# Performance work log

Hardware: AMD Instinct MI355X
Metric: run time of the kernel (lower is better)

Reference implementation:

```python
import jax, jax.numpy as jnp
import numpy as np

# dims
N = 32768      # nodes
E = 1048576    # edges (avg degree 32)
DIN = 64       # input scalar dim
NS = 64        # 0e multiplicity of hidden irreps
NV = 32        # 1o multiplicity of hidden irreps
LAT = 256      # config.LATENT_DIM_GNN
L = 2          # n_layers
S3 = 1.0 / np.sqrt(3.0)  # CG coefficient for 1o x 1o -> 0e (dot / sqrt(3))


def setup_inputs() -> dict:
    key = jax.random.key(0)
    ks = jax.random.split(key, 20)
    p = lambda k, s: jax.random.normal(k, s, jnp.float32)
    return {
        "x": p(ks[0], (N, DIN)),
        "edge_attr": p(ks[2], (E, 4)),            # [rel_vec(3) | dist(1)] = 1x1o + 1x0e
        "W_in": p(ks[3], (DIN, NS)),              # initial e3nn Linear: only 0e->0e connects
        "W_out": p(ks[4], (NS, LAT)),             # final projection on scalar irreps
        "W_ss": p(ks[5], (L, NS, NS)),            # message TP: 0e x 0e -> 0e
        "W_vv0": p(ks[6], (L, NV, NS)),           # message TP: 1o x 1o -> 0e
        "W_sv": p(ks[7], (L, NS, NV)),            # message TP: 0e x 1o -> 1o
        "W_vs": p(ks[8], (L, NV, NV)),            # message TP: 1o x 0e -> 1o
        "gm_w": p(ks[9], (L, NV * 3)), "gm_b": p(ks[10], (L, NV * 3)),
        "W_uss": p(ks[11], (L, NS, NS, NS)),      # update TP: 0e x 0e -> 0e
        "W_uvv": p(ks[12], (L, NV, NV, NS)),      # update TP: 1o x 1o -> 0e
        "W_usv": p(ks[13], (L, NS, NV, NV)),      # update TP: 0e x 1o -> 1o
        "W_uvs": p(ks[14], (L, NV, NS, NV)),      # update TP: 1o x 0e -> 1o
        "gu_w": p(ks[15], (L, NV * 3)), "gu_b": p(ks[16], (L, NV * 3)),
        "edge_index": jax.random.randint(ks[1], (2, E), 0, N),
    }


def _gate(s, v, gw, gb):
    # RobustGate manual path: silu on scalars; vectors gated by
    # sigmoid(Linear(mean over nonscalar dims)) broadcast over the flattened block.
    s = jax.nn.silu(s)
    vf = v.reshape(v.shape[0], -1)                       # [*, NV*3]
    g = jax.nn.sigmoid(vf.mean(-1, keepdims=True) * gw + gb)
    return s, (vf * g).reshape(v.shape)


def reference(x, edge_attr, W_in, W_out, W_ss, W_vv0, W_sv, W_vs, gm_w, gm_b,
              W_uss, W_uvv, W_usv, W_uvs, gu_w, gu_b, edge_index):
    row, col = edge_index[0], edge_index[1]
    ev, es = edge_attr[:, :3], edge_attr[:, 3]           # 1x1o, 1x0e edge attrs
    # initial projection 64x0e -> 64x0e + 32x1o (vector part starts at zero)
    ns = x @ W_in / np.sqrt(DIN)                         # [N, NS]
    nv = jnp.zeros((x.shape[0], NV, 3), x.dtype)         # [N, NV, 3]
    r2 = np.sqrt(2.0)
    for l in range(L):
        # ---- message: gather -> FullyConnectedTensorProduct(node, edge) ----
        hs, hv = ns[col], nv[col]
        m_s = (jnp.einsum('ei,io->eo', hs * es[:, None], W_ss[l]) / np.sqrt(NS)
               + jnp.einsum('emx,ex,mo->eo', hv, ev, W_vv0[l]) * S3 / np.sqrt(NV)) / r2
        m_v = (jnp.einsum('ei,ex,im->emx', hs, ev, W_sv[l]) / np.sqrt(NS)
               + jnp.einsum('emx,mn->enx', hv * es[:, None, None], W_vs[l]) / np.sqrt(NV)) / r2
        m_s, m_v = _gate(m_s, m_v, gm_w[l], gm_b[l])
        # ---- scatter-add aggregation ----
        a_s = jax.ops.segment_sum(m_s, row, num_segments=N)
        a_v = jax.ops.segment_sum(m_v, row, num_segments=N)
        # ---- update: FullyConnectedTensorProduct(node, aggregated) ----
        u_s = (jnp.einsum('ei,ej,ijo->eo', ns, a_s, W_uss[l]) / NS
               + jnp.einsum('emx,enx,mno->eo', nv, a_v, W_uvv[l]) * S3 / NV) / r2
        u_v = (jnp.einsum('ei,enx,ino->eox', ns, a_v, W_usv[l]) / np.sqrt(NS * NV)
               + jnp.einsum('emx,ej,mjo->eox', nv, a_s, W_uvs[l]) / np.sqrt(NS * NV)) / r2
        u_s, u_v = _gate(u_s, u_v, gu_w[l], gu_b[l])
        # residual node update
        ns = ns + u_s
        nv = nv + u_v
    # extract scalar (l=0) features, final projection to LAT x 0e
    return ns @ W_out / np.sqrt(NS)
```

## Files before the change

kernel.cpp:

```cpp
#include <hip/hip_runtime.h>

#define N_NODES 32768
#define N_EDGES 1048576
#define PREP_L  467968

typedef short bfrag8 __attribute__((ext_vector_type(8)));
typedef float f32x4  __attribute__((ext_vector_type(4)));

#define MFMA(a,b,c) __builtin_amdgcn_mfma_f32_16x16x32_bf16(a,b,c,0,0,0)

__device__ __forceinline__ short f2bf(float f){
    unsigned u = __float_as_uint(f);
    u += 0x7fffu + ((u >> 16) & 1u);
    return (short)(u >> 16);
}
__device__ __forceinline__ float bf2f(short s){
    return __uint_as_float(((unsigned)(unsigned short)s) << 16);
}
__device__ __forceinline__ float sigm(float x){ return 1.0f/(1.0f + __expf(-x)); }
__device__ __forceinline__ float siluf(float x){ return x * sigm(x); }

__global__ void k_prep(const float* Wss, const float* Wvv0, const float* Wsv,
                       const float* Wvs, const float* Wuss, const float* Wuvv,
                       const float* Wusv, const float* Wuvs, const float* Wout,
                       short* wp)
{
    int idx = blockIdx.x*256 + threadIdx.x;
    const int total = 2*PREP_L + 16384;
    if (idx >= total) return;
    const float s_ss  = 0.0883883476483f;
    const float s_vv  = 0.0721687836487f;
    const float s_sv  = 0.0883883476483f;
    const float s_vs  = 0.125f;
    const float s_uss = 0.0110485434560f;
    const float s_uvv = 0.0127577593310f;
    const float s_uvw = 0.015625f;
    float v;
    if (idx >= 2*PREP_L){
        int r = idx - 2*PREP_L; int o = r >> 6, i = r & 63;
        v = Wout[i*256 + o] * 0.125f;
    } else {
        int l = idx / PREP_L; int off = idx - l*PREP_L;
        if (off < 6144){ int o = off/96, k = off - o*96;
            v = (k < 64) ? Wss[l*4096 + k*64 + o]*s_ss
                         : Wvv0[l*2048 + (k-64)*64 + o]*s_vv;
        } else if (off < 8192){ int tt = off - 6144; int m = tt>>6, i = tt&63;
            v = Wsv[l*2048 + i*32 + m]*s_sv;
        } else if (off < 9216){ int tt = off - 8192; int n = tt>>5, m = tt&31;
            v = Wvs[l*1024 + m*32 + n]*s_vs;
        } else if (off < 336896){ int tt = off - 9216; int o = tt/5120, k = tt - o*5120;
            if (k < 4096) v = Wuss[l*262144 + k*64 + o]*s_uss;
            else          v = Wuvv[l*65536 + (k-4096)*64 + o]*s_uvv;
        } else if (off < 402432){ int tt = off - 336896; int nf = tt>>6, i = tt&63;
            int n = nf>>5, o = nf&31;
            v = Wusv[l*65536 + i*1024 + n*32 + o]*s_uvw;
        } else { int tt = off - 402432; int nf = tt>>6, j = tt&63;
            int m = nf>>5, o = nf&31;
            v = Wuvs[l*65536 + m*2048 + j*32 + o]*s_uvw;
        }
    }
    wp[idx] = f2bf(v);
}

__global__ void k_in(const float* __restrict__ x, const float* __restrict__ Win,
                     float* __restrict__ ns)
{
    int wv = threadIdx.x >> 6, o = threadIdx.x & 63;
    int node = blockIdx.x*4 + wv;
    const float* xr = x + (size_t)node*64;
    float acc = 0.f;
    #pragma unroll
    for (int i=0;i<64;i++) acc += xr[i]*Win[i*64+o];
    ns[(size_t)node*64+o] = 0.125f*acc;
}

__global__ void k_pack(const float* __restrict__ ns, const float* __restrict__ nv,
                       short* __restrict__ nsbf, short* __restrict__ nvbf)
{
    int t = threadIdx.x;
    int nb = blockIdx.x*16;
    for (int idx=t; idx<1024; idx+=256){
        int nd = idx>>6, i = idx&63;
        nsbf[(size_t)(nb+nd)*64 + i] = f2bf(ns[(size_t)(nb+nd)*64 + i]);
    }
    for (int idx=t; idx<1536; idx+=256){
        int nd = idx/96, r = idx - nd*96;
        int x = r>>5, m = r&31;
        nvbf[((size_t)x<<20) + (size_t)(nb+nd)*32 + m] = f2bf(nv[(size_t)(nb+nd)*96 + m*3 + x]);
    }
}

__global__ void k_hist(const int* __restrict__ eidx, int* __restrict__ cnt)
{
    int e = blockIdx.x*256 + threadIdx.x;
    atomicAdd(&cnt[eidx[e]], 1);
}

__global__ void k_scan(const int* __restrict__ cnt, int* __restrict__ cursor)
{
    __shared__ int part[256];
    int t = threadIdx.x;
    int base = t*128;
    int s = 0;
    for (int i=0;i<128;i++) s += cnt[base+i];
    part[t] = s; __syncthreads();
    for (int off=1; off<256; off<<=1){
        int v = (t>=off) ? part[t-off] : 0;
        __syncthreads();
        part[t] += v;
        __syncthreads();
    }
    int run = part[t] - s;
    for (int i=0;i<128;i++){ cursor[base+i] = run; run += cnt[base+i]; }
}

__global__ void k_scatter(const int* __restrict__ eidx, const float* __restrict__ eattr,
                          int* __restrict__ cursor, int* __restrict__ col_s,
                          int* __restrict__ row_s, float4* __restrict__ ea_s)
{
    int e = blockIdx.x*256 + threadIdx.x;
    int r = eidx[e];
    int d = atomicAdd(&cursor[r], 1);
    row_s[d] = r;
    col_s[d] = eidx[N_EDGES + e];
    ea_s[d]  = ((const float4*)eattr)[e];
}

__global__ __launch_bounds__(256, 3) void k_edge(
        const short* __restrict__ nsbf, const short* __restrict__ nvbf,
        const int* __restrict__ col_s, const int* __restrict__ row_s,
        const float4* __restrict__ ea_s,
        const short* __restrict__ wp_l,
        const float* __restrict__ gmw, const float* __restrict__ gmb,
        float* __restrict__ a_s, float* __restrict__ a_v)
{
    __shared__ __align__(16) short sA1[4][16*36];
    __shared__ __align__(16) short sA2[4][16*72];
    __shared__ __align__(16) short sAv[4][3*16*36];
    __shared__ int    sRow[4][16];
    __shared__ float4 sEv4[4][16];
    __shared__ float  sAcc[24*160];

    const int t = threadIdx.x;
    const int w = t >> 6, lane = t & 63;
    const int col = lane & 15, quad = lane >> 4;
    const int blockStart = blockIdx.x*256;
    const int rfirst = row_s[blockStart];

    for (int i=t; i<24*160; i+=256) sAcc[i] = 0.f;

    const short* W1t  = wp_l;
    const short* Wsvt = wp_l + 6144;
    const short* Wvst = wp_l + 8192;

    bfrag8 bss[2][4], bvv[4], bsv[2][2], bvs[2];
    #pragma unroll
    for (int s=0;s<2;s++)
        #pragma unroll
        for (int nt=0;nt<4;nt++)
            bss[s][nt] = *(const bfrag8*)(W1t + (nt*16+col)*96 + s*32 + quad*8);
    #pragma unroll
    for (int nt=0;nt<4;nt++)
        bvv[nt] = *(const bfrag8*)(W1t + (nt*16+col)*96 + 64 + quad*8);
    #pragma unroll
    for (int s=0;s<2;s++)
        #pragma unroll
        for (int nt=0;nt<2;nt++)
            bsv[s][nt] = *(const bfrag8*)(Wsvt + (nt*16+col)*64 + s*32 + quad*8);
    #pragma unroll
    for (int nt=0;nt<2;nt++)
        bvs[nt] = *(const bfrag8*)(Wvst + (nt*16+col)*32 + quad*8);

    float gwv[2][3], gbv[2][3];
    #pragma unroll
    for (int h=0;h<2;h++)
        #pragma unroll
        for (int xx=0;xx<3;xx++){
            int k = (h*16+col)*3+xx;
            gwv[h][xx] = gmw[k]; gbv[h][xx] = gmb[k];
        }

    auto emit = [&](int r, int f, float v){
        int rl = r - rfirst;
        if (rl < 24) atomicAdd(&sAcc[rl*160 + f], v);
        else if (f < 64) atomicAdd(&a_s[(size_t)r*64 + f], v);
        else             atomicAdd(&a_v[(size_t)r*96 + f - 64], v);
    };

    __syncthreads();

    for (int it=0; it<4; it++){
        int tileBase = blockStart + w*64 + it*16;
        {
            int e = col, q = quad;
            int sg = tileBase + e;
            int c = col_s[sg];
            float4 ea = ea_s[sg];
            const short* hsrc = nsbf + (size_t)c*64 + q*16;
            bfrag8 h0 = *(const bfrag8*)(hsrc);
            bfrag8 h1 = *(const bfrag8*)(hsrc + 8);
            *(bfrag8*)&sA2[w][e*72 + q*16]     = h0;
            *(bfrag8*)&sA2[w][e*72 + q*16 + 8] = h1;
            bfrag8 av[3];
            #pragma unroll
            for (int xx=0;xx<3;xx++){
                av[xx] = *(const bfrag8*)(nvbf + ((size_t)xx<<20) + (size_t)c*32 + q*8);
                *(bfrag8*)&sAv[w][xx*576 + e*36 + q*8] = av[xx];
            }
            bfrag8 vt;
            #pragma unroll
            for (int mi=0;mi<8;mi++)
                vt[mi] = f2bf(bf2f(av[0][mi])*ea.x + bf2f(av[1][mi])*ea.y + bf2f(av[2][mi])*ea.z);
            *(bfrag8*)&sA1[w][e*36 + q*8] = vt;
            if (q==0){
                sRow[w][e] = row_s[sg];
                sEv4[w][e] = ea;
            }
        }
        __syncthreads();
        f32x4 accss[4], accvv[4], accp[2], accq[3][2];
        #pragma unroll
        for (int nt=0;nt<4;nt++){ accss[nt] = (f32x4){0.f,0.f,0.f,0.f};
                                  accvv[nt] = (f32x4){0.f,0.f,0.f,0.f}; }
        #pragma unroll
        for (int nt=0;nt<2;nt++) accp[nt] = (f32x4){0.f,0.f,0.f,0.f};
        #pragma unroll
        for (int xx=0;xx<3;xx++)
            #pragma unroll
            for (int nt=0;nt<2;nt++) accq[xx][nt] = (f32x4){0.f,0.f,0.f,0.f};
        {
            bfrag8 a1 = *(bfrag8*)&sA1[w][col*36 + quad*8];
            bfrag8 a20 = *(bfrag8*)&sA2[w][col*72 + quad*8];
            bfrag8 a21 = *(bfrag8*)&sA2[w][col*72 + 32 + quad*8];
            #pragma unroll
            for (int nt=0;nt<4;nt++) accss[nt] = MFMA(a20, bss[0][nt], accss[nt]);
            #pragma unroll
            for (int nt=0;nt<4;nt++) accss[nt] = MFMA(a21, bss[1][nt], accss[nt]);
            #pragma unroll
            for (int nt=0;nt<4;nt++) accvv[nt] = MFMA(a1, bvv[nt], accvv[nt]);
            #pragma unroll
            for (int nt=0;nt<2;nt++) accp[nt] = MFMA(a20, bsv[0][nt], accp[nt]);
            #pragma unroll
            for (int nt=0;nt<2;nt++) accp[nt] = MFMA(a21, bsv[1][nt], accp[nt]);
            #pragma unroll
            for (int xx=0;xx<3;xx++){
                bfrag8 avx = *(bfrag8*)&sAv[w][xx*576 + col*36 + quad*8];
                #pragma unroll
                for (int nt=0;nt<2;nt++) accq[xx][nt] = MFMA(avx, bvs[nt], accq[xx][nt]);
            }
        }

        float4 ev4[4];
        #pragma unroll
        for (int reg=0;reg<4;reg++) ev4[reg] = sEv4[w][quad*4+reg];
        float mean[4];
        #pragma unroll
        for (int reg=0;reg<4;reg++){
            float es = ev4[reg].w;
            float part = 0.f;
            #pragma unroll
            for (int h=0;h<2;h++){
                part += accp[h][reg]*ev4[reg].x + es*accq[0][h][reg];
                part += accp[h][reg]*ev4[reg].y + es*accq[1][h][reg];
                part += accp[h][reg]*ev4[reg].z + es*accq[2][h][reg];
            }
            part += __shfl_xor(part,1); part += __shfl_xor(part,2);
            part += __shfl_xor(part,4); part += __shfl_xor(part,8);
            mean[reg] = part*(1.0f/96.0f);
        }

        int r0 = sRow[w][0], r15 = sRow[w][15];
        bool uni = (r0 == r15);
        int rq[4];
        #pragma unroll
        for (int reg=0;reg<4;reg++) rq[reg] = sRow[w][quad*4+reg];
        bool c1 = rq[1]==rq[0], c2 = rq[2]==rq[1], c3 = rq[3]==rq[2];
        auto out4 = [&](int f, float v0, float v1, float v2, float v3){
            if (uni){
                float s = v0+v1+v2+v3;
                s += __shfl_xor(s,16); s += __shfl_xor(s,32);
                if (quad==0) emit(r0, f, s);
            } else {
                float run = v0;
                if (c1) run += v1; else { emit(rq[0], f, run); run = v1; }
                if (c2) run += v2; else { emit(rq[1], f, run); run = v2; }
                if (c3) run += v3; else { emit(rq[2], f, run); run = v3; }
                emit(rq[3], f, run);
            }
        };
        #pragma unroll
        for (int nt=0;nt<4;nt++){
            float v[4];
            #pragma unroll
            for (int reg=0;reg<4;reg++)
                v[reg] = siluf(ev4[reg].w*accss[nt][reg] + accvv[nt][reg]);
            out4(nt*16+col, v[0], v[1], v[2], v[3]);
        }
        #pragma unroll
        for (int h=0;h<2;h++)
            #pragma unroll
            for (int xx=0;xx<3;xx++){
                float v[4];
                #pragma unroll
                for (int reg=0;reg<4;reg++){
                    float evx = (xx==0) ? ev4[reg].x : ((xx==1) ? ev4[reg].y : ev4[reg].z);
                    float val = accp[h][reg]*evx + ev4[reg].w*accq[xx][h][reg];
                    v[reg] = val * sigm(mean[reg]*gwv[h][xx] + gbv[h][xx]);
                }
                out4(64 + (h*16+col)*3+xx, v[0], v[1], v[2], v[3]);
            }
        __syncthreads();
    }

    int rlast = row_s[blockStart + 255];
    int nr = rlast - rfirst + 1; if (nr > 24) nr = 24;
    for (int i=t; i<nr*160; i+=256){
        float v = sAcc[i];
        if (v != 0.f){
            int rl = i/160, f = i - rl*160;
            int r = rfirst + rl;
            if (f < 64) atomicAdd(&a_s[(size_t)r*64 + f], v);
            else        atomicAdd(&a_v[(size_t)r*96 + f - 64], v);
        }
    }
}

__global__ __launch_bounds__(256) void k_us(
        const float* __restrict__ ns, const float* __restrict__ nvv,
        const float* __restrict__ a_s, const float* __restrict__ a_v,
        const short* __restrict__ Wusst, float* __restrict__ ns_out)
{
    __shared__ __align__(16) float ns16[16*68];
    __shared__ __align__(16) float as16[16*68];
    __shared__ __align__(16) float nv16[16*100];
    __shared__ __align__(16) float av16[16*100];
    __shared__ __align__(16) short sA[16*1032];

    const int t = threadIdx.x;
    const int w = t>>6, lane = t&63, col = lane&15, quad = lane>>4;
    const int nb = blockIdx.x*16;

    for (int idx=t; idx<1024; idx+=256){ int nd = idx>>6, i = idx&63;
        ns16[nd*68+i] = ns[(size_t)(nb+nd)*64+i];
        as16[nd*68+i] = a_s[(size_t)(nb+nd)*64+i];
    }
    for (int idx=t; idx<1536; idx+=256){ int nd = idx/96, i = idx-nd*96;
        nv16[nd*100+i] = nvv[(size_t)(nb+nd)*96+i];
        av16[nd*100+i] = a_v[(size_t)(nb+nd)*96+i];
    }
    __syncthreads();

    f32x4 acc = {0.f,0.f,0.f,0.f};
    for (int c=0;c<5;c++){
        if (c) __syncthreads();
        if (c < 4){
            #pragma unroll
            for (int itg=0; itg<8; itg++){
                int rid = t + itg*256;
                int nd = rid & 15;
                int kk0 = (rid>>4)<<3;
                int i = (c<<4) + (kk0>>6);
                int j0 = kk0 & 63;
                float nsv = ns16[nd*68 + i];
                const float* ap = &as16[nd*68 + j0];
                float4 x0 = *(const float4*)ap;
                float4 x1 = *(const float4*)(ap+4);
                bfrag8 o8;
                o8[0]=f2bf(nsv*x0.x); o8[1]=f2bf(nsv*x0.y); o8[2]=f2bf(nsv*x0.z); o8[3]=f2bf(nsv*x0.w);
                o8[4]=f2bf(nsv*x1.x); o8[5]=f2bf(nsv*x1.y); o8[6]=f2bf(nsv*x1.z); o8[7]=f2bf(nsv*x1.w);
                *(bfrag8*)&sA[nd*1032 + kk0] = o8;
            }
        } else {
            #pragma unroll
            for (int itg=0; itg<8; itg++){
                int rid = t + itg*256;
                int nd = rid & 15;
                int kk0 = (rid>>4)<<3;
                int m = kk0>>5, n0 = kk0&31;
                float v0 = nv16[nd*100 + m*3];
                float v1 = nv16[nd*100 + m*3+1];
                float v2 = nv16[nd*100 + m*3+2];
                const float* vp = &av16[nd*100 + n0*3];
                float yf[24];
                #pragma unroll
                for (int a=0;a<6;a++){ float4 y = *(const float4*)(vp+4*a);
                    yf[4*a]=y.x; yf[4*a+1]=y.y; yf[4*a+2]=y.z; yf[4*a+3]=y.w; }
                bfrag8 o8;
                #pragma unroll
                for (int jj=0;jj<8;jj++)
                    o8[jj] = f2bf(v0*yf[jj*3] + v1*yf[jj*3+1] + v2*yf[jj*3+2]);
                *(bfrag8*)&sA[nd*1032 + kk0] = o8;
            }
        }
        __syncthreads();
        const short* bp = Wusst + (size_t)(w*16+col)*5120 + c*1024 + quad*8;
        #pragma unroll
        for (int s=0;s<32;s++){
            bfrag8 a = *(bfrag8*)&sA[col*1032 + s*32 + quad*8];
            bfrag8 b = *(const bfrag8*)(bp + s*32);
            acc = MFMA(a, b, acc);
        }
    }
    #pragma unroll
    for (int reg=0; reg<4; reg++){
        int nd = quad*4 + reg;
        int o = w*16 + col;
        ns_out[(size_t)(nb+nd)*64 + o] = ns16[nd*68 + o] + siluf(acc[reg]);
    }
}

__global__ __launch_bounds__(256) void k_uv(
        const float* __restrict__ ns, const float* __restrict__ nvv,
        const float* __restrict__ a_s, const float* __restrict__ a_v,
        const short* __restrict__ Wusvt, const short* __restrict__ Wuvst,
        const float* __restrict__ guw, const float* __restrict__ gub,
        float* __restrict__ nv_out)
{
    __shared__ __align__(16) short nsbf[16*72];
    __shared__ __align__(16) short asbf[16*72];
    __shared__ __align__(16) float nv16[16*100];
    __shared__ __align__(16) float av16[16*100];
    __shared__ float uvb[2][16][96];

    const int t = threadIdx.x;
    const int w = t>>6, lane = t&63, col = lane&15, quad = lane>>4;
    const int nb = blockIdx.x*16;

    for (int idx=t; idx<1024; idx+=256){ int nd = idx>>6, i = idx&63;
        nsbf[nd*72+i] = f2bf(ns[(size_t)(nb+nd)*64+i]);
        asbf[nd*72+i] = f2bf(a_s[(size_t)(nb+nd)*64+i]);
    }
    for (int idx=t; idx<1536; idx+=256){ int nd = idx/96, i = idx-nd*96;
        nv16[nd*100+i] = nvv[(size_t)(nb+nd)*96+i];
        av16[nd*100+i] = a_v[(size_t)(nb+nd)*96+i];
    }
    __syncthreads();

    const int h = w>>1, o0 = (w&1)*16;
    const short* src = h ? asbf : nsbf;
    bfrag8 a0 = *(bfrag8*)&src[col*72 + quad*8];
    bfrag8 a1 = *(bfrag8*)&src[col*72 + 32 + quad*8];
    const short* Bt = h ? Wuvst : Wusvt;
    const float* M  = h ? nv16 : av16;
    float uva[3][4] = {};
    for (int n=0;n<32;n++){
        f32x4 acc = {0.f,0.f,0.f,0.f};
        const short* bp = Bt + (size_t)((n<<5) + o0 + col)*64 + quad*8;
        bfrag8 b0 = *(const bfrag8*)(bp);
        bfrag8 b1 = *(const bfrag8*)(bp + 32);
        acc = MFMA(a0,b0,acc);
        acc = MFMA(a1,b1,acc);
        #pragma unroll
        for (int reg=0;reg<4;reg++){
            int nd = quad*4+reg;
            float m0 = M[nd*100 + n*3];
            float m1 = M[nd*100 + n*3+1];
            float m2 = M[nd*100 + n*3+2];
            uva[0][reg] += acc[reg]*m0;
            uva[1][reg] += acc[reg]*m1;
            uva[2][reg] += acc[reg]*m2;
        }
    }
    #pragma unroll
    for (int reg=0;reg<4;reg++){
        int nd = quad*4+reg;
        #pragma unroll
        for (int xx=0;xx<3;xx++)
            uvb[h][nd][(o0+col)*3+xx] = uva[xx][reg];
    }
    __syncthreads();
    {
        int nd = t>>4, j = t&15;
        float part = 0.f;
        #pragma unroll
        for (int kk=j; kk<96; kk+=16) part += uvb[0][nd][kk] + uvb[1][nd][kk];
        part += __shfl_xor(part,1); part += __shfl_xor(part,2);
        part += __shfl_xor(part,4); part += __shfl_xor(part,8);
        float mean = part*(1.0f/96.0f);
        #pragma unroll
        for (int q2=0;q2<6;q2++){
            int kk = j*6 + q2;
            float uv = uvb[0][nd][kk] + uvb[1][nd][kk];
            float g = sigm(mean*guw[kk] + gub[kk]);
            nv_out[(size_t)(nb+nd)*96 + kk] = nv16[nd*100+kk] + uv*g;
        }
    }
}

__global__ __launch_bounds__(256) void k_out(const float* __restrict__ ns,
                                             const short* __restrict__ Woutt,
                                             float* __restrict__ outp)
{
    __shared__ __align__(16) short nsbf[16*72];
    const int t = threadIdx.x;
    const int w = t>>6, lane = t&63, col = lane&15, quad = lane>>4;
    const int nb = blockIdx.x*16;
    for (int idx=t; idx<1024; idx+=256){ int nd=idx>>6, i=idx&63;
        nsbf[nd*72+i] = f2bf(ns[(size_t)(nb+nd)*64+i]); }
    __syncthreads();
    bfrag8 a0 = *(bfrag8*)&nsbf[col*72 + quad*8];
    bfrag8 a1 = *(bfrag8*)&nsbf[col*72 + 32 + quad*8];
    #pragma unroll
    for (int nt=0;nt<4;nt++){
        int o = w*64 + nt*16 + col;
        const short* bp = Woutt + (size_t)o*64 + quad*8;
        bfrag8 b0 = *(const bfrag8*)bp;
        bfrag8 b1 = *(const bfrag8*)(bp+32);
        f32x4 acc = {0.f,0.f,0.f,0.f};
        acc = MFMA(a0,b0,acc);
        acc = MFMA(a1,b1,acc);
        #pragma unroll
        for (int reg=0;reg<4;reg++)
            outp[(size_t)(nb + quad*4+reg)*256 + o] = acc[reg];
    }
}

extern "C" void kernel_launch(void* const* d_in, const int* in_sizes, int n_in,
                              void* d_out, int out_size, void* d_ws, size_t ws_size,
                              hipStream_t stream)
{
    const float* x     = (const float*)d_in[0];
    const float* eattr = (const float*)d_in[1];
    const float* Win   = (const float*)d_in[2];
    const float* Wout  = (const float*)d_in[3];
    const float* Wss   = (const float*)d_in[4];
    const float* Wvv0  = (const float*)d_in[5];
    const float* Wsv   = (const float*)d_in[6];
    const float* Wvs   = (const float*)d_in[7];
    const float* gmw   = (const float*)d_in[8];
    const float* gmb   = (const float*)d_in[9];
    const float* Wuss  = (const float*)d_in[10];
    const float* Wuvv  = (const float*)d_in[11];
    const float* Wusv  = (const float*)d_in[12];
    const float* Wuvs  = (const float*)d_in[13];
    const float* guw   = (const float*)d_in[14];
    const float* gub   = (const float*)d_in[15];
    const int*   eidx  = (const int*)d_in[16];
    float* outp = (float*)d_out;

    char* p = (char*)d_ws;
    float* ns_a = (float*)p; p += (size_t)N_NODES*64*4;
    float* ns_b = (float*)p; p += (size_t)N_NODES*64*4;
    float* nv_a = (float*)p; p += (size_t)N_NODES*96*4;
    float* nv_b = (float*)p; p += (size_t)N_NODES*96*4;
    float* a_s  = (float*)p; p += (size_t)N_NODES*64*4;
    float* a_v  = (float*)p; p += (size_t)N_NODES*96*4;
    int*   cnt    = (int*)p;   p += (size_t)N_NODES*4;
    int*   cursor = (int*)p;   p += (size_t)N_NODES*4;
    int*   col_s  = (int*)p;   p += (size_t)N_EDGES*4;
    int*   row_s  = (int*)p;   p += (size_t)N_EDGES*4;
    float4* ea_s  = (float4*)p; p += (size_t)N_EDGES*16;
    short* wp   = (short*)p;   p += (size_t)(2*PREP_L + 16384)*2;
    short* nsbf = (short*)p;   p += (size_t)N_NODES*64*2;
    short* nvbf = (short*)p;   p += (size_t)3*N_NODES*32*2;

    k_prep<<<3720, 256, 0, stream>>>(Wss,Wvv0,Wsv,Wvs,Wuss,Wuvv,Wusv,Wuvs,Wout,wp);
    hipMemsetAsync(nv_a, 0, (size_t)N_NODES*96*4, stream);
    hipMemsetAsync(cnt, 0, (size_t)N_NODES*4, stream);
    k_in<<<N_NODES/4, 256, 0, stream>>>(x, Win, ns_a);
    k_hist<<<N_EDGES/256, 256, 0, stream>>>(eidx, cnt);
    k_scan<<<1, 256, 0, stream>>>(cnt, cursor);
    k_scatter<<<N_EDGES/256, 256, 0, stream>>>(eidx, eattr, cursor, col_s, row_s, ea_s);

    for (int l=0;l<2;l++){
        const float* cns = l ? ns_b : ns_a;
        const float* cnv = l ? nv_b : nv_a;
        float* nns = l ? ns_a : ns_b;
        float* nnv = l ? nv_a : nv_b;
        k_pack<<<N_NODES/16, 256, 0, stream>>>(cns, cnv, nsbf, nvbf);
        hipMemsetAsync(a_s, 0, (size_t)N_NODES*(64+96)*4, stream);
        k_edge<<<N_EDGES/256, 256, 0, stream>>>(nsbf, nvbf, col_s, row_s, ea_s,
                                         wp + (size_t)l*PREP_L,
                                         gmw + l*96, gmb + l*96, a_s, a_v);
        k_uv<<<N_NODES/16, 256, 0, stream>>>(cns, cnv, a_s, a_v,
                                             wp + (size_t)l*PREP_L + 336896,
                                             wp + (size_t)l*PREP_L + 402432,
                                             guw + l*96, gub + l*96, nnv);
        k_us<<<N_NODES/16, 256, 0, stream>>>(cns, cnv, a_s, a_v,
                                             wp + (size_t)l*PREP_L + 9216, nns);
    }
    k_out<<<N_NODES/16, 256, 0, stream>>>(ns_a, wp + (size_t)2*PREP_L, outp);
}
```

Baseline: 1.391 ms.

## Partition edge kernel by destination-node ranges via CSR row pointers, drop global atomics

The edge kernel now assigns each block a fixed range of 8 destination nodes, using a CSR row_ptr built in the scan kernel, instead of a fixed 256-edge chunk. All aggregation goes to shared memory and is written out once with plain stores, so the global atomics and the per-layer memset of a_s and a_v are no longer needed. The per-tile __syncthreads calls are removed because each wave only touches its own shared staging buffers. In exchange, per-block work now depends on node degree, so load can be uneven, and partial tiles need masking, which wastes some MFMA work on padded edges.

```diff
diff --git a/kernel.cpp b/kernel.cpp
--- a/kernel.cpp
+++ b/kernel.cpp
@@ -96,7 +96,8 @@
     atomicAdd(&cnt[eidx[e]], 1);
 }
 
-__global__ void k_scan(const int* __restrict__ cnt, int* __restrict__ cursor)
+__global__ void k_scan(const int* __restrict__ cnt, int* __restrict__ cursor,
+                       int* __restrict__ row_ptr)
 {
     __shared__ int part[256];
     int t = threadIdx.x;
@@ -111,7 +112,8 @@
         __syncthreads();
     }
     int run = part[t] - s;
-    for (int i=0;i<128;i++){ cursor[base+i] = run; run += cnt[base+i]; }
+    for (int i=0;i<128;i++){ cursor[base+i] = run; row_ptr[base+i] = run; run += cnt[base+i]; }
+    if (t == 255) row_ptr[N_NODES] = N_EDGES;
 }
 
 __global__ void k_scatter(const int* __restrict__ eidx, const float* __restrict__ eattr,
@@ -129,7 +131,7 @@
 __global__ __launch_bounds__(256, 3) void k_edge(
         const short* __restrict__ nsbf, const short* __restrict__ nvbf,
         const int* __restrict__ col_s, const int* __restrict__ row_s,
-        const float4* __restrict__ ea_s,
+        const float4* __restrict__ ea_s, const int* __restrict__ row_ptr,
         const short* __restrict__ wp_l,
         const float* __restrict__ gmw, const float* __restrict__ gmb,
         float* __restrict__ a_s, float* __restrict__ a_v)
@@ -139,15 +141,15 @@
     __shared__ __align__(16) short sAv[4][3*16*36];
     __shared__ int    sRow[4][16];
     __shared__ float4 sEv4[4][16];
-    __shared__ float  sAcc[24*160];
+    __shared__ float  sAcc[8*160];
 
     const int t = threadIdx.x;
     const int w = t >> 6, lane = t & 63;
     const int col = lane & 15, quad = lane >> 4;
-    const int blockStart = blockIdx.x*256;
-    const int rfirst = row_s[blockStart];
-
-    for (int i=t; i<24*160; i+=256) sAcc[i] = 0.f;
+    const int r0 = blockIdx.x*8;
+    const int e0 = row_ptr[r0], e1 = row_ptr[r0+8];
+
+    for (int i=t; i<8*160; i+=256) sAcc[i] = 0.f;
 
     const short* W1t  = wp_l;
     const short* Wsvt = wp_l + 6144;
@@ -180,22 +182,18 @@
             gwv[h][xx] = gmw[k]; gbv[h][xx] = gmb[k];
         }
 
-    auto emit = [&](int r, int f, float v){
-        int rl = r - rfirst;
-        if (rl < 24) atomicAdd(&sAcc[rl*160 + f], v);
-        else if (f < 64) atomicAdd(&a_s[(size_t)r*64 + f], v);
-        else             atomicAdd(&a_v[(size_t)r*96 + f - 64], v);
-    };
-
     __syncthreads();
 
-    for (int it=0; it<4; it++){
-        int tileBase = blockStart + w*64 + it*16;
+    const int ntiles = (e1 - e0 + 15) >> 4;
+    for (int tid=w; tid<ntiles; tid+=4){
         {
             int e = col, q = quad;
-            int sg = tileBase + e;
-            int c = col_s[sg];
-            float4 ea = ea_s[sg];
+            int sg = e0 + tid*16 + e;
+            bool valid = sg < e1;
+            int sgc = valid ? sg : (e1-1);
+            int c = col_s[sgc];
+            float4 ea = ea_s[sgc];
+            if (!valid){ ea.x=0.f; ea.y=0.f; ea.z=0.f; ea.w=0.f; }
             const short* hsrc = nsbf + (size_t)c*64 + q*16;
             bfrag8 h0 = *(const bfrag8*)(hsrc);
             bfrag8 h1 = *(const bfrag8*)(hsrc + 8);
@@ -213,11 +211,10 @@
                 vt[mi] = f2bf(bf2f(av[0][mi])*ea.x + bf2f(av[1][mi])*ea.y + bf2f(av[2][mi])*ea.z);
             *(bfrag8*)&sA1[w][e*36 + q*8] = vt;
             if (q==0){
-                sRow[w][e] = row_s[sg];
+                sRow[w][e] = row_s[sgc] - r0;
                 sEv4[w][e] = ea;
             }
         }
-        __syncthreads();
         f32x4 accss[4], accvv[4], accp[2], accq[3][2];
         #pragma unroll
         for (int nt=0;nt<4;nt++){ accss[nt] = (f32x4){0.f,0.f,0.f,0.f};
@@ -269,8 +266,8 @@
             mean[reg] = part*(1.0f/96.0f);
         }
 
-        int r0 = sRow[w][0], r15 = sRow[w][15];
-        bool uni = (r0 == r15);
+        int rl0 = sRow[w][0], rl15 = sRow[w][15];
+        bool uni = (rl0 == rl15);
         int rq[4];
         #pragma unroll
         for (int reg=0;reg<4;reg++) rq[reg] = sRow[w][quad*4+reg];
@@ -279,13 +276,13 @@
             if (uni){
                 float s = v0+v1+v2+v3;
                 s += __shfl_xor(s,16); s += __shfl_xor(s,32);
-                if (quad==0) emit(r0, f, s);
+                if (quad==0) atomicAdd(&sAcc[rl0*160 + f], s);
             } else {
                 float run = v0;
-                if (c1) run += v1; else { emit(rq[0], f, run); run = v1; }
-                if (c2) run += v2; else { emit(rq[1], f, run); run = v2; }
-                if (c3) run += v3; else { emit(rq[2], f, run); run = v3; }
-                emit(rq[3], f, run);
+                if (c1) run += v1; else { atomicAdd(&sAcc[rq[0]*160 + f], run); run = v1; }
+                if (c2) run += v2; else { atomicAdd(&sAcc[rq[1]*160 + f], run); run = v2; }
+                if (c3) run += v3; else { atomicAdd(&sAcc[rq[2]*160 + f], run); run = v3; }
+                atomicAdd(&sAcc[rq[3]*160 + f], run);
             }
         };
         #pragma unroll
@@ -309,19 +306,15 @@
                 }
                 out4(64 + (h*16+col)*3+xx, v[0], v[1], v[2], v[3]);
             }
-        __syncthreads();
-    }
-
-    int rlast = row_s[blockStart + 255];
-    int nr = rlast - rfirst + 1; if (nr > 24) nr = 24;
-    for (int i=t; i<nr*160; i+=256){
+    }
+
+    __syncthreads();
+    for (int i=t; i<8*160; i+=256){
+        int rl = i/160, f = i - rl*160;
+        int r = r0 + rl;
         float v = sAcc[i];
-        if (v != 0.f){
-            int rl = i/160, f = i - rl*160;
-            int r = rfirst + rl;
-            if (f < 64) atomicAdd(&a_s[(size_t)r*64 + f], v);
-            else        atomicAdd(&a_v[(size_t)r*96 + f - 64], v);
-        }
+        if (f < 64) a_s[(size_t)r*64 + f] = v;
+        else        a_v[(size_t)r*96 + f - 64] = v;
     }
 }
 
@@ -545,11 +538,12 @@
     float* nv_b = (float*)p; p += (size_t)N_NODES*96*4;
     float* a_s  = (float*)p; p += (size_t)N_NODES*64*4;
     float* a_v  = (float*)p; p += (size_t)N_NODES*96*4;
-    int*   cnt    = (int*)p;   p += (size_t)N_NODES*4;
-    int*   cursor = (int*)p;   p += (size_t)N_NODES*4;
-    int*   col_s  = (int*)p;   p += (size_t)N_EDGES*4;
-    int*   row_s  = (int*)p;   p += (size_t)N_EDGES*4;
-    float4* ea_s  = (float4*)p; p += (size_t)N_EDGES*16;
+    int*   cnt     = (int*)p;   p += (size_t)N_NODES*4;
+    int*   cursor  = (int*)p;   p += (size_t)N_NODES*4;
+    int*   row_ptr = (int*)p;   p += (size_t)(N_NODES+1)*4;
+    int*   col_s   = (int*)p;   p += (size_t)N_EDGES*4;
+    int*   row_s   = (int*)p;   p += (size_t)N_EDGES*4;
+    float4* ea_s   = (float4*)p; p += (size_t)N_EDGES*16;
     short* wp   = (short*)p;   p += (size_t)(2*PREP_L + 16384)*2;
     short* nsbf = (short*)p;   p += (size_t)N_NODES*64*2;
     short* nvbf = (short*)p;   p += (size_t)3*N_NODES*32*2;
@@ -559,7 +553,7 @@
     hipMemsetAsync(cnt, 0, (size_t)N_NODES*4, stream);
     k_in<<<N_NODES/4, 256, 0, stream>>>(x, Win, ns_a);
     k_hist<<<N_EDGES/256, 256, 0, stream>>>(eidx, cnt);
-    k_scan<<<1, 256, 0, stream>>>(cnt, cursor);
+    k_scan<<<1, 256, 0, stream>>>(cnt, cursor, row_ptr);
     k_scatter<<<N_EDGES/256, 256, 0, stream>>>(eidx, eattr, cursor, col_s, row_s, ea_s);
 
     for (int l=0;l<2;l++){
@@ -568,8 +562,7 @@
         float* nns = l ? ns_a : ns_b;
         float* nnv = l ? nv_a : nv_b;
         k_pack<<<N_NODES/16, 256, 0, stream>>>(cns, cnv, nsbf, nvbf);
-        hipMemsetAsync(a_s, 0, (size_t)N_NODES*(64+96)*4, stream);
-        k_edge<<<N_EDGES/256, 256, 0, stream>>>(nsbf, nvbf, col_s, row_s, ea_s,
+        k_edge<<<N_NODES/8, 256, 0, stream>>>(nsbf, nvbf, col_s, row_s, ea_s, row_ptr,
                                          wp + (size_t)l*PREP_L,
                                          gmw + l*96, gmb + l*96, a_s, a_v);
         k_uv<<<N_NODES/16, 256, 0, stream>>>(cns, cnv, a_s, a_v,
```

Result: faster. 1.323 ms (-4.9%).
